# Kernel optimization log

Measured on AMD Instinct MI355X. Metric: run time of the kernel, lower is better.

## Reference

```python
import jax, jax.numpy as jnp
import numpy as np

# Model dims
T0 = 2048      # tokens (batch*seq flattened)
D = 2048       # hidden_size
E = 256        # n_routed_experts
K = 8          # num_experts_per_tok
G = 8          # expert groups
EG = 32        # experts per group
R = 64         # tucker rank
I = 1408       # moe_intermediate_size


def setup_inputs() -> dict:
    key = jax.random.key(0)
    ks = jax.random.split(key, 12)
    f = lambda k, s: jax.random.normal(k, s, dtype=jnp.float32) * 0.02
    return {
        "hidden_states": jax.random.normal(ks[0], (T0, D), dtype=jnp.float32),
        "w_gate": f(ks[1], (D, E)),
        # Tucker factors per group: shared in-factor A, per-expert core C, shared out-factor B
        "A_gate": f(ks[2], (G, D, R)), "C_gate": f(ks[3], (G, EG, R, R)), "B_gate": f(ks[4], (G, R, I)),
        "A_up":   f(ks[5], (G, D, R)), "C_up":   f(ks[6], (G, EG, R, R)), "B_up":   f(ks[7], (G, R, I)),
        "A_down": f(ks[8], (G, I, R)), "C_down": f(ks[9], (G, EG, R, R)), "B_down": f(ks[10], (G, R, D)),
    }


def _tucker(x, A, C, B, inner):
    # x: [T, d_in], A: [d_in, R], C: [EG, R, R] gathered per-token, B: [R, d_out]
    h1 = x @ A                                    # [T, R]
    h2 = jnp.einsum('tr,trs->ts', h1, C[inner])   # per-token expert core
    return h2 @ B                                 # [T, d_out]


def reference(hidden_states, w_gate, A_gate, C_gate, B_gate,
              A_up, C_up, B_up, A_down, C_down, B_down):
    # Router: softmax in fp32, top-k, renormalize
    logits = hidden_states @ w_gate                              # [T0, E]
    probs = jax.nn.softmax(logits.astype(jnp.float32), axis=-1)
    rw, sel = jax.lax.top_k(probs, K)                            # [T0, K]
    rw = (rw / rw.sum(axis=-1, keepdims=True)).astype(hidden_states.dtype)

    idx = sel.reshape(-1)          # [T0*K] expert ids of dispatched rows
    gid = idx // EG                # group id
    inner = idx % EG               # expert within group
    x = jnp.repeat(hidden_states, K, axis=0)   # repeat_interleave dispatch [T0*K, D]

    out = jnp.zeros_like(x)
    for g in range(G):             # static loop over 8 structurally distinct groups
        m = (gid == g)[:, None]
        xg = jnp.where(m, x, 0.0)  # masked dispatch (zeros flow to zero through the MLP)
        go = _tucker(xg, A_gate[g], C_gate[g], B_gate[g], inner)
        uo = _tucker(xg, A_up[g],   C_up[g],   B_up[g],   inner)
        inter = jax.nn.silu(go) * uo
        do = _tucker(inter, A_down[g], C_down[g], B_down[g], inner)
        out = out + jnp.where(m, do, 0.0)

    # weighted combine
    return (out.reshape(T0, K, D) * rw[..., None]).sum(axis=1)
```

## Files before the change

### kernel.cpp

```cpp
#include <hip/hip_runtime.h>
#include <math.h>

constexpr int T0n = 2048;
constexpr int Dn  = 2048;
constexpr int En  = 256;
constexpr int Gn  = 8;
constexpr int EGn = 32;
constexpr int Rn  = 64;
constexpr int In  = 1408;

constexpr int NROWS = T0n * 8;
constexpr int SEGCAP = NROWS;
constexpr int KSPLIT = 4;

typedef __attribute__((ext_vector_type(8))) short s8v;
typedef __attribute__((ext_vector_type(4))) float f4v;
#define MFMA16(a, b, c) __builtin_amdgcn_mfma_f32_16x16x32_bf16(a, b, c, 0, 0, 0)

__device__ __forceinline__ unsigned short f2bf(float x) {
  unsigned int u = __float_as_uint(x);
  unsigned int r = (u + 0x7FFFu + ((u >> 16) & 1u)) >> 16;
  return (unsigned short)r;
}

struct TD { const float* src; unsigned short* dst; int rows, cols, nbx, per_batch, base; };
struct TD6 { TD t[6]; };

__global__ __launch_bounds__(256) void k_tcvt6(TD6 D) {
  __shared__ float tbuf[32][33];
  int id = blockIdx.x;
  int ti = 0;
#pragma unroll
  for (int i = 1; i < 6; ++i) ti = (id >= D.t[i].base) ? i : ti;
  TD d = D.t[ti];
  int local = id - d.base;
  int bz = local / d.per_batch;
  int rem = local - bz * d.per_batch;
  int by = rem / d.nbx;
  int bx = rem - by * d.nbx;

  size_t boff = (size_t)bz * d.rows * d.cols;
  const float* src = d.src + boff;
  unsigned short* dst = d.dst + boff;
  int c0 = bx * 32, r0 = by * 32;
  int tx = threadIdx.x & 31, ty = threadIdx.x >> 5;
  for (int i = ty; i < 32; i += 8)
    tbuf[i][tx] = src[(size_t)(r0 + i) * d.cols + c0 + tx];
  __syncthreads();
  for (int i = ty; i < 32; i += 8)
    dst[(size_t)(c0 + i) * d.rows + r0 + tx] = f2bf(tbuf[tx][i]);
}

__global__ __launch_bounds__(256) void k_router_part(
    const float* __restrict__ A, const float* __restrict__ B,
    double* __restrict__ part, unsigned short* __restrict__ Hb) {
  __shared__ double Asd[32][66];
  __shared__ double Bsd[32][66];
  const int m0 = blockIdx.y * 64, n0 = blockIdx.x * 64;
  const int kbeg = blockIdx.z * (Dn / KSPLIT);
  const int tid = threadIdx.x;
  const int ty = tid >> 4, tx = tid & 15;
  const int lm = tid & 63, lk8 = (tid >> 6) * 8;
  const int br = tid >> 3, bc = (tid & 7) * 8;
  const bool emitH = (blockIdx.x == 0);

  double acc[4][4] = {};

  for (int k0 = kbeg; k0 < kbeg + Dn / KSPLIT; k0 += 32) {
    float4 a0 = *(const float4*)&A[(size_t)(m0 + lm) * Dn + k0 + lk8];
    float4 a1 = *(const float4*)&A[(size_t)(m0 + lm) * Dn + k0 + lk8 + 4];
    Asd[lk8 + 0][lm] = (double)a0.x; Asd[lk8 + 1][lm] = (double)a0.y;
    Asd[lk8 + 2][lm] = (double)a0.z; Asd[lk8 + 3][lm] = (double)a0.w;
    Asd[lk8 + 4][lm] = (double)a1.x; Asd[lk8 + 5][lm] = (double)a1.y;
    Asd[lk8 + 6][lm] = (double)a1.z; Asd[lk8 + 7][lm] = (double)a1.w;
    if (emitH) {
      ushort4 o0, o1;
      o0.x = f2bf(a0.x); o0.y = f2bf(a0.y); o0.z = f2bf(a0.z); o0.w = f2bf(a0.w);
      o1.x = f2bf(a1.x); o1.y = f2bf(a1.y); o1.z = f2bf(a1.z); o1.w = f2bf(a1.w);
      *(ushort4*)&Hb[(size_t)(m0 + lm) * Dn + k0 + lk8] = o0;
      *(ushort4*)&Hb[(size_t)(m0 + lm) * Dn + k0 + lk8 + 4] = o1;
    }
    float4 b0 = *(const float4*)&B[(size_t)(k0 + br) * En + n0 + bc];
    float4 b1 = *(const float4*)&B[(size_t)(k0 + br) * En + n0 + bc + 4];
    Bsd[br][bc + 0] = (double)b0.x; Bsd[br][bc + 1] = (double)b0.y;
    Bsd[br][bc + 2] = (double)b0.z; Bsd[br][bc + 3] = (double)b0.w;
    Bsd[br][bc + 4] = (double)b1.x; Bsd[br][bc + 5] = (double)b1.y;
    Bsd[br][bc + 6] = (double)b1.z; Bsd[br][bc + 7] = (double)b1.w;
    __syncthreads();
#pragma unroll
    for (int kk = 0; kk < 32; ++kk) {
      double a[4], b[4];
#pragma unroll
      for (int i = 0; i < 4; ++i) a[i] = Asd[kk][ty + 16 * i];
#pragma unroll
      for (int j = 0; j < 4; ++j) b[j] = Bsd[kk][tx + 16 * j];
#pragma unroll
      for (int i = 0; i < 4; ++i)
#pragma unroll
        for (int j = 0; j < 4; ++j)
          acc[i][j] += a[i] * b[j];
    }
    __syncthreads();
  }
  double* prow = part + (size_t)blockIdx.z * T0n * En;
#pragma unroll
  for (int i = 0; i < 4; ++i) {
    int row = m0 + ty + 16 * i;
#pragma unroll
    for (int j = 0; j < 4; ++j)
      prow[(size_t)row * En + n0 + tx + 16 * j] = acc[i][j];
  }
}

__global__ __launch_bounds__(256) void k_topk(
    const double* __restrict__ part, int* __restrict__ sel,
    float* __restrict__ rw, int* __restrict__ cnt_e) {
  const int wid = threadIdx.x >> 6, ln = threadIdx.x & 63;
  const int t = blockIdx.x * 4 + wid;

  double v[4];
#pragma unroll
  for (int j = 0; j < 4; ++j) {
    double s = 0.0;
#pragma unroll
    for (int kc = 0; kc < KSPLIT; ++kc)
      s += part[((size_t)kc * T0n + t) * En + ln + 64 * j];
    v[j] = s;
  }

  float topv[8];
  int topi[8];
#pragma unroll
  for (int k = 0; k < 8; ++k) {
    double bv = v[0]; int bi = ln;
#pragma unroll
    for (int j = 1; j < 4; ++j) {
      int cand = ln + 64 * j;
      if (v[j] > bv || (v[j] == bv && cand < bi)) { bv = v[j]; bi = cand; }
    }
#pragma unroll
    for (int off = 32; off > 0; off >>= 1) {
      double ov = __shfl_xor(bv, off);
      int oi = __shfl_xor(bi, off);
      if (ov > bv || (ov == bv && oi < bi)) { bv = ov; bi = oi; }
    }
    topv[k] = (float)bv; topi[k] = bi;
    if ((bi & 63) == ln) v[bi >> 6] = -1e300;
  }

  if (ln < 8) {
    float m = topv[0];
    float ssum = 0.f;
#pragma unroll
    for (int k = 0; k < 8; ++k) ssum += expf(topv[k] - m);
    rw[t * 8 + ln] = expf(topv[ln] - m) / ssum;
    sel[t * 8 + ln] = topi[ln];
    atomicAdd(&cnt_e[topi[ln]], 1);
  }
}

__global__ __launch_bounds__(256) void k_scan(
    const int* __restrict__ cnt_e, int* __restrict__ off_e,
    int* __restrict__ cur_e, int* __restrict__ grp_n) {
  __shared__ int c[256];
  int tid = threadIdx.x;
  c[tid] = cnt_e[tid];
  __syncthreads();
  int g = tid >> 5, ei = tid & 31;
  int run = 0;
  for (int i = 0; i < ei; ++i) run += c[(g << 5) + i];
  off_e[tid] = g * SEGCAP + run;
  cur_e[tid] = g * SEGCAP + run;
  if (ei == 31) grp_n[g] = run + c[tid];
}

__global__ void k_scatter(const int* __restrict__ sel, int* __restrict__ cur_e,
                          int* __restrict__ rseg) {
  int i = blockIdx.x * 256 + threadIdx.x;
  int e = sel[i];
  int pos = atomicAdd(&cur_e[e], 1);
  rseg[pos] = i;
}

__global__ __launch_bounds__(512) void k_h1_mfma(
    const unsigned short* __restrict__ Hb,
    const unsigned short* __restrict__ AgT, const unsigned short* __restrict__ AuT,
    unsigned short* __restrict__ h1gb, unsigned short* __restrict__ h1ub) {
  const int t0 = blockIdx.x * 64;
  const int g = blockIdx.y;
  const unsigned short* Wg = AgT + (size_t)g * Rn * Dn;
  const unsigned short* Wu = AuT + (size_t)g * Rn * Dn;

  __shared__ unsigned short As[64 * 72];
  __shared__ unsigned short Bg_l[64 * 72];
  __shared__ unsigned short Bu_l[64 * 72];
  const int tid = threadIdx.x;
  const int w = tid >> 6, ln = tid & 63;
  const int path = w >> 2, ws = w & 3;
  const int quad = ln >> 4, lane16 = ln & 15;
  const int j = tid >> 3, q = (tid & 7) * 8;

  f4v S[4] = {};

  for (int k0 = 0; k0 < Dn; k0 += 64) {
    *(uint4*)&As[j * 72 + q]   = *(const uint4*)&Hb[(size_t)(t0 + j) * Dn + k0 + q];
    *(uint4*)&Bg_l[j * 72 + q] = *(const uint4*)&Wg[(size_t)j * Dn + k0 + q];
    *(uint4*)&Bu_l[j * 72 + q] = *(const uint4*)&Wu[(size_t)j * Dn + k0 + q];
    __syncthreads();
    const unsigned short* Bl = path ? Bu_l : Bg_l;
#pragma unroll
    for (int kk = 0; kk < 2; ++kk) {
      s8v a = *(const s8v*)&As[(ws * 16 + lane16) * 72 + kk * 32 + quad * 8];
#pragma unroll
      for (int nt = 0; nt < 4; ++nt) {
        s8v b = *(const s8v*)&Bl[(nt * 16 + lane16) * 72 + kk * 32 + quad * 8];
        S[nt] = MFMA16(a, b, S[nt]);
      }
    }
    __syncthreads();
  }
  unsigned short* out = path ? h1ub : h1gb;
#pragma unroll
  for (int nt = 0; nt < 4; ++nt)
#pragma unroll
    for (int r = 0; r < 4; ++r) {
      int row = t0 + ws * 16 + quad * 4 + r;
      int col = g * 64 + nt * 16 + lane16;
      out[(size_t)row * (Gn * Rn) + col] = f2bf(S[nt][r]);
    }
}

__global__ __launch_bounds__(512) void k_core_gu(
    const unsigned short* __restrict__ h1gb, const unsigned short* __restrict__ h1ub,
    const float* __restrict__ Cgate, const float* __restrict__ Cup,
    const int* __restrict__ rseg, const int* __restrict__ off_e,
    const int* __restrict__ cnt_e,
    unsigned short* __restrict__ h2gb, unsigned short* __restrict__ h2ub) {
  const int e = blockIdx.x;
  const int ne = cnt_e[e];
  if (ne == 0) return;
  const int g = e >> 5;
  const int base = off_e[e];
  __shared__ unsigned short Cg_l[64 * 72];
  __shared__ unsigned short Cu_l[64 * 72];
  __shared__ unsigned short Ags[64 * 72];
  __shared__ unsigned short Aus[64 * 72];
  __shared__ int rids[64];
  const int tid = threadIdx.x;
  const int w = tid >> 6, ln = tid & 63;
  const int path = w >> 2, ws = w & 3;
  const int quad = ln >> 4, lane16 = ln & 15;
  const int j = tid >> 3, q = (tid & 7) * 8;
  {
    const float* cg = Cgate + (size_t)e * (Rn * Rn);
    const float* cu = Cup   + (size_t)e * (Rn * Rn);
    float4 g0 = *(const float4*)&cg[j * 64 + q];
    float4 g1 = *(const float4*)&cg[j * 64 + q + 4];
    float4 u0 = *(const float4*)&cu[j * 64 + q];
    float4 u1 = *(const float4*)&cu[j * 64 + q + 4];
    Cg_l[(q + 0) * 72 + j] = f2bf(g0.x); Cg_l[(q + 1) * 72 + j] = f2bf(g0.y);
    Cg_l[(q + 2) * 72 + j] = f2bf(g0.z); Cg_l[(q + 3) * 72 + j] = f2bf(g0.w);
    Cg_l[(q + 4) * 72 + j] = f2bf(g1.x); Cg_l[(q + 5) * 72 + j] = f2bf(g1.y);
    Cg_l[(q + 6) * 72 + j] = f2bf(g1.z); Cg_l[(q + 7) * 72 + j] = f2bf(g1.w);
    Cu_l[(q + 0) * 72 + j] = f2bf(u0.x); Cu_l[(q + 1) * 72 + j] = f2bf(u0.y);
    Cu_l[(q + 2) * 72 + j] = f2bf(u0.z); Cu_l[(q + 3) * 72 + j] = f2bf(u0.w);
    Cu_l[(q + 4) * 72 + j] = f2bf(u1.x); Cu_l[(q + 5) * 72 + j] = f2bf(u1.y);
    Cu_l[(q + 6) * 72 + j] = f2bf(u1.z); Cu_l[(q + 7) * 72 + j] = f2bf(u1.w);
  }
  const int ntile = (ne + 63) >> 6;
  for (int it = 0; it < ntile; ++it) {
    int mi = it * 64 + j;
    int rid = (mi < ne) ? rseg[base + mi] : -1;
    if ((tid & 7) == 0) rids[j] = rid;
    uint4 zg = {0, 0, 0, 0}, zu = {0, 0, 0, 0};
    if (rid >= 0) {
      zg = *(const uint4*)&h1gb[(size_t)(rid >> 3) * (Gn * Rn) + g * 64 + q];
      zu = *(const uint4*)&h1ub[(size_t)(rid >> 3) * (Gn * Rn) + g * 64 + q];
    }
    *(uint4*)&Ags[j * 72 + q] = zg;
    *(uint4*)&Aus[j * 72 + q] = zu;
    __syncthreads();
    const unsigned short* Al = path ? Aus : Ags;
    const unsigned short* Cl = path ? Cu_l : Cg_l;
    f4v S[4] = {};
#pragma unroll
    for (int kk = 0; kk < 2; ++kk) {
      s8v a = *(const s8v*)&Al[(ws * 16 + lane16) * 72 + kk * 32 + quad * 8];
#pragma unroll
      for (int nt = 0; nt < 4; ++nt) {
        s8v b = *(const s8v*)&Cl[(nt * 16 + lane16) * 72 + kk * 32 + quad * 8];
        S[nt] = MFMA16(a, b, S[nt]);
      }
    }
    unsigned short* out = path ? h2ub : h2gb;
#pragma unroll
    for (int nt = 0; nt < 4; ++nt)
#pragma unroll
      for (int r = 0; r < 4; ++r) {
        int rid2 = rids[ws * 16 + quad * 4 + r];
        if (rid2 >= 0)
          out[(size_t)rid2 * 64 + nt * 16 + lane16] = f2bf(S[nt][r]);
      }
    __syncthreads();
  }
}

__global__ __launch_bounds__(256) void k_expand_mfma(
    const unsigned short* __restrict__ h2gb, const unsigned short* __restrict__ h2ub,
    const unsigned short* __restrict__ BgT, const unsigned short* __restrict__ BuT,
    const unsigned short* __restrict__ AdT,
    const int* __restrict__ rseg, const int* __restrict__ grp_n,
    float* __restrict__ h1d) {
  const int g = blockIdx.z;
  const int ng = grp_n[g];
  const int m0 = blockIdx.y * 128;
  if (m0 >= ng) return;
  const int c_beg = blockIdx.x * 6;
  const int c_end = min(22, c_beg + 6);

  __shared__ unsigned short Hg_l[128 * 72];
  __shared__ unsigned short Hu_l[128 * 72];
  __shared__ unsigned short Bg_l[64 * 72];
  __shared__ unsigned short Bu_l[64 * 72];
  __shared__ unsigned short Ad_l[64 * 72];
  __shared__ int rids[128];

  const int tid = threadIdx.x;
  const int w = tid >> 6, ln = tid & 63;
  const int quad = ln >> 4, lane16 = ln & 15;

  if (tid < 128) rids[tid] = (m0 + tid < ng) ? rseg[g * SEGCAP + m0 + tid] : -1;
  __syncthreads();
#pragma unroll
  for (int i = 0; i < 4; ++i) {
    int c = tid + i * 256;
    int row = c >> 3, cc = (c & 7) * 8;
    int rid = rids[row];
    uint4 zg = {0, 0, 0, 0}, zu = {0, 0, 0, 0};
    if (rid >= 0) {
      zg = *(const uint4*)&h2gb[(size_t)rid * 64 + cc];
      zu = *(const uint4*)&h2ub[(size_t)rid * 64 + cc];
    }
    *(uint4*)&Hg_l[row * 72 + cc] = zg;
    *(uint4*)&Hu_l[row * 72 + cc] = zu;
  }

  const unsigned short* Bg_base = BgT + (size_t)g * In * Rn;
  const unsigned short* Bu_base = BuT + (size_t)g * In * Rn;
  const unsigned short* Ad_base = AdT + (size_t)g * Rn * In;

  f4v P[2][4] = {};

  for (int c = c_beg; c < c_end; ++c) {
    const int i0 = c * 64;
#pragma unroll
    for (int i = 0; i < 2; ++i) {
      int cq = tid + i * 256;
      int row = cq >> 3, co = (cq & 7) * 8;
      *(uint4*)&Bg_l[row * 72 + co] = *(const uint4*)&Bg_base[(size_t)(i0 + row) * Rn + co];
      *(uint4*)&Bu_l[row * 72 + co] = *(const uint4*)&Bu_base[(size_t)(i0 + row) * Rn + co];
      *(uint4*)&Ad_l[row * 72 + co] = *(const uint4*)&Ad_base[(size_t)row * In + i0 + co];
    }
    __syncthreads();

    f4v Sg[2][4] = {}, Su[2][4] = {};
#pragma unroll
    for (int kk = 0; kk < 2; ++kk) {
      s8v ag[2], au[2], bg[4], bu[4];
#pragma unroll
      for (int mt = 0; mt < 2; ++mt) {
        ag[mt] = *(const s8v*)&Hg_l[(w * 32 + mt * 16 + lane16) * 72 + kk * 32 + quad * 8];
        au[mt] = *(const s8v*)&Hu_l[(w * 32 + mt * 16 + lane16) * 72 + kk * 32 + quad * 8];
      }
#pragma unroll
      for (int nt = 0; nt < 4; ++nt) {
        bg[nt] = *(const s8v*)&Bg_l[(nt * 16 + lane16) * 72 + kk * 32 + quad * 8];
        bu[nt] = *(const s8v*)&Bu_l[(nt * 16 + lane16) * 72 + kk * 32 + quad * 8];
      }
#pragma unroll
      for (int mt = 0; mt < 2; ++mt)
#pragma unroll
        for (int nt = 0; nt < 4; ++nt) {
          Sg[mt][nt] = MFMA16(ag[mt], bg[nt], Sg[mt][nt]);
          Su[mt][nt] = MFMA16(au[mt], bu[nt], Su[mt][nt]);
        }
    }
    __syncthreads();
    {
      unsigned short* ibuf = (w < 2) ? Bg_l : Bu_l;
#pragma unroll
      for (int mt = 0; mt < 2; ++mt)
#pragma unroll
        for (int nt = 0; nt < 4; ++nt)
#pragma unroll
          for (int r = 0; r < 4; ++r) {
            float sg = Sg[mt][nt][r];
            float v = sg / (1.f + __expf(-sg)) * Su[mt][nt][r];
            int row = (w * 32 + mt * 16 + quad * 4 + r) & 63;
            ibuf[row * 72 + nt * 16 + lane16] = f2bf(v);
          }
    }
    __syncthreads();
#pragma unroll
    for (int kk = 0; kk < 2; ++kk) {
      s8v ai[2], bd[4];
#pragma unroll
      for (int mt = 0; mt < 2; ++mt) {
        const unsigned short* src = (w < 2) ? Bg_l : Bu_l;
        int arow = (w * 32 + mt * 16 + lane16) & 63;
        ai[mt] = *(const s8v*)&src[arow * 72 + kk * 32 + quad * 8];
      }
#pragma unroll
      for (int nt = 0; nt < 4; ++nt)
        bd[nt] = *(const s8v*)&Ad_l[(nt * 16 + lane16) * 72 + kk * 32 + quad * 8];
#pragma unroll
      for (int mt = 0; mt < 2; ++mt)
#pragma unroll
        for (int nt = 0; nt < 4; ++nt)
          P[mt][nt] = MFMA16(ai[mt], bd[nt], P[mt][nt]);
    }
    __syncthreads();
  }

#pragma unroll
  for (int mt = 0; mt < 2; ++mt)
#pragma unroll
    for (int nt = 0; nt < 4; ++nt)
#pragma unroll
      for (int r = 0; r < 4; ++r) {
        int lrow = w * 32 + mt * 16 + quad * 4 + r;
        int rid = rids[lrow];
        if (rid >= 0)
          atomicAdd(&h1d[(size_t)rid * 64 + nt * 16 + lane16], P[mt][nt][r]);
      }
}

__global__ __launch_bounds__(512) void k_core_down(
    const float* __restrict__ h1d, const float* __restrict__ Cdown,
    const float* __restrict__ rw,
    const int* __restrict__ rseg, const int* __restrict__ off_e,
    const int* __restrict__ cnt_e,
    float* __restrict__ y) {
  const int e = blockIdx.x;
  const int ne = cnt_e[e];
  if (ne == 0) return;
  const int g = e >> 5;
  const int base = off_e[e];
  __shared__ unsigned short Bd_l[64 * 72];
  __shared__ unsigned short Ad_l[128 * 72];
  __shared__ int rids[128];
  const int tid = threadIdx.x;
  const int w = tid >> 6, ln = tid & 63;
  const int quad = ln >> 4, lane16 = ln & 15;
  {
    int j = tid >> 3, q = (tid & 7) * 8;
    const float* cd = Cdown + (size_t)e * (Rn * Rn);
    float4 d0 = *(const float4*)&cd[j * 64 + q];
    float4 d1 = *(const float4*)&cd[j * 64 + q + 4];
    Bd_l[(q + 0) * 72 + j] = f2bf(d0.x); Bd_l[(q + 1) * 72 + j] = f2bf(d0.y);
    Bd_l[(q + 2) * 72 + j] = f2bf(d0.z); Bd_l[(q + 3) * 72 + j] = f2bf(d0.w);
    Bd_l[(q + 4) * 72 + j] = f2bf(d1.x); Bd_l[(q + 5) * 72 + j] = f2bf(d1.y);
    Bd_l[(q + 6) * 72 + j] = f2bf(d1.z); Bd_l[(q + 7) * 72 + j] = f2bf(d1.w);
  }
  const int gj = tid >> 2, gq = (tid & 3) * 16;
  const int ntile = (ne + 127) >> 7;
  for (int it = 0; it < ntile; ++it) {
    int mi = it * 128 + gj;
    int rid = (mi < ne) ? rseg[base + mi] : -1;
    if ((tid & 3) == 0) rids[gj] = rid;
#pragma unroll
    for (int i = 0; i < 4; ++i) {
      int kb = gq + i * 4;
      float4 vd = {0.f, 0.f, 0.f, 0.f};
      if (rid >= 0) vd = *(const float4*)&h1d[(size_t)rid * 64 + kb];
      ushort4 od;
      od.x = f2bf(vd.x); od.y = f2bf(vd.y); od.z = f2bf(vd.z); od.w = f2bf(vd.w);
      *(ushort4*)&Ad_l[gj * 72 + kb] = od;
    }
    __syncthreads();
    f4v Sd[4] = {};
#pragma unroll
    for (int kk = 0; kk < 2; ++kk) {
      s8v ad = *(const s8v*)&Ad_l[(w * 16 + lane16) * 72 + kk * 32 + quad * 8];
#pragma unroll
      for (int nt = 0; nt < 4; ++nt) {
        s8v bd = *(const s8v*)&Bd_l[(nt * 16 + lane16) * 72 + kk * 32 + quad * 8];
        Sd[nt] = MFMA16(ad, bd, Sd[nt]);
      }
    }
#pragma unroll
    for (int nt = 0; nt < 4; ++nt)
#pragma unroll
      for (int r = 0; r < 4; ++r) {
        int rid2 = rids[w * 16 + quad * 4 + r];
        if (rid2 >= 0) {
          float wgt = rw[rid2];
          atomicAdd(&y[(size_t)(rid2 >> 3) * (Gn * Rn) + g * 64 + nt * 16 + lane16],
                    wgt * Sd[nt][r]);
        }
      }
    __syncthreads();
  }
}

__global__ __launch_bounds__(256) void k_combine(
    const float* __restrict__ y, const unsigned short* __restrict__ BdT,
    float* __restrict__ outp) {
  const int t0 = blockIdx.y * 128, n0 = blockIdx.x * 128;
  __shared__ unsigned short As[128 * 72];
  __shared__ unsigned short Bs[128 * 72];
  const int tid = threadIdx.x;
  const int w = tid >> 6, ln = tid & 63;
  const int quad = ln >> 4, lane16 = ln & 15;
  const int mbase = (w >> 1) * 64, nbase = (w & 1) * 64;

  f4v acc[4][4] = {};

  for (int k0 = 0; k0 < Gn * Rn; k0 += 64) {
#pragma unroll
    for (int i = 0; i < 8; ++i) {
      int c = tid + i * 256;
      int row = c >> 4, cc = (c & 15) * 4;
      float4 v = *(const float4*)&y[(size_t)(t0 + row) * (Gn * Rn) + k0 + cc];
      ushort4 o;
      o.x = f2bf(v.x); o.y = f2bf(v.y); o.z = f2bf(v.z); o.w = f2bf(v.w);
      *(ushort4*)&As[row * 72 + cc] = o;
    }
#pragma unroll
    for (int i = 0; i < 4; ++i) {
      int c = tid + i * 256;
      int row = c >> 3, cc = (c & 7) * 8;
      *(uint4*)&Bs[row * 72 + cc] = *(const uint4*)&BdT[(size_t)(n0 + row) * (Gn * Rn) + k0 + cc];
    }
    __syncthreads();
#pragma unroll
    for (int kk = 0; kk < 2; ++kk) {
      s8v a[4], b[4];
#pragma unroll
      for (int mt = 0; mt < 4; ++mt)
        a[mt] = *(const s8v*)&As[(mbase + mt * 16 + lane16) * 72 + kk * 32 + quad * 8];
#pragma unroll
      for (int nt = 0; nt < 4; ++nt)
        b[nt] = *(const s8v*)&Bs[(nbase + nt * 16 + lane16) * 72 + kk * 32 + quad * 8];
#pragma unroll
      for (int mt = 0; mt < 4; ++mt)
#pragma unroll
        for (int nt = 0; nt < 4; ++nt)
          acc[mt][nt] = MFMA16(a[mt], b[nt], acc[mt][nt]);
    }
    __syncthreads();
  }
#pragma unroll
  for (int mt = 0; mt < 4; ++mt)
#pragma unroll
    for (int nt = 0; nt < 4; ++nt)
#pragma unroll
      for (int r = 0; r < 4; ++r)
        outp[(size_t)(t0 + mbase + mt * 16 + quad * 4 + r) * Dn +
             n0 + nbase + nt * 16 + lane16] = acc[mt][nt][r];
}

extern "C" void kernel_launch(void* const* d_in, const int* in_sizes, int n_in,
                              void* d_out, int out_size, void* d_ws, size_t ws_size,
                              hipStream_t stream) {
  const float* hidden = (const float*)d_in[0];
  const float* w_gate = (const float*)d_in[1];
  const float* A_gate = (const float*)d_in[2];
  const float* C_gate = (const float*)d_in[3];
  const float* B_gate = (const float*)d_in[4];
  const float* A_up   = (const float*)d_in[5];
  const float* C_up   = (const float*)d_in[6];
  const float* B_up   = (const float*)d_in[7];
  const float* A_down = (const float*)d_in[8];
  const float* C_down = (const float*)d_in[9];
  const float* B_down = (const float*)d_in[10];
  float* out = (float*)d_out;

  char* base = (char*)d_ws;
  double* part = (double*)d_ws;
  size_t o = 0;
  unsigned short* h2gb = (unsigned short*)(base + o); o += (size_t)NROWS * Rn * 2;
  unsigned short* h2ub = (unsigned short*)(base + o); o += (size_t)NROWS * Rn * 2;
  unsigned short* h1gb = (unsigned short*)(base + o); o += (size_t)T0n * Gn * Rn * 2;
  unsigned short* h1ub = (unsigned short*)(base + o); o += (size_t)T0n * Gn * Rn * 2;
  float* h1d = (float*)(base + o); o += (size_t)NROWS * Rn * 4;
  float* y   = (float*)(base + o); o += (size_t)T0n * Gn * Rn * 4;
  unsigned short* Hb  = (unsigned short*)(base + o); o += (size_t)T0n * Dn * 2;
  unsigned short* AgT = (unsigned short*)(base + o); o += (size_t)Gn * Rn * Dn * 2;
  unsigned short* AuT = (unsigned short*)(base + o); o += (size_t)Gn * Rn * Dn * 2;
  unsigned short* BgT = (unsigned short*)(base + o); o += (size_t)Gn * In * Rn * 2;
  unsigned short* BuT = (unsigned short*)(base + o); o += (size_t)Gn * In * Rn * 2;
  unsigned short* AdT = (unsigned short*)(base + o); o += (size_t)Gn * Rn * In * 2;
  unsigned short* BdT = (unsigned short*)(base + o); o += (size_t)Dn * Gn * Rn * 2;
  float* rwp = (float*)(base + o); o += (size_t)NROWS * 4;
  int* sel   = (int*)(base + o); o += (size_t)NROWS * 4;
  int* rseg  = (int*)(base + o); o += (size_t)Gn * SEGCAP * 4;
  int* cnt_e = (int*)(base + o); o += En * 4;
  int* off_e = (int*)(base + o); o += En * 4;
  int* cur_e = (int*)(base + o); o += En * 4;
  int* grp_n = (int*)(base + o); o += Gn * 4;

  hipMemsetAsync(cnt_e, 0, En * sizeof(int), stream);

  k_router_part<<<dim3(En / 64, T0n / 64, KSPLIT), 256, 0, stream>>>(
      hidden, w_gate, part, Hb);
  k_topk<<<T0n / 4, 256, 0, stream>>>(part, sel, rwp, cnt_e);
  k_scan<<<1, 256, 0, stream>>>(cnt_e, off_e, cur_e, grp_n);
  k_scatter<<<NROWS / 256, 256, 0, stream>>>(sel, cur_e, rseg);

  hipMemsetAsync(h1d, 0, (size_t)(NROWS * Rn + T0n * Gn * Rn) * sizeof(float), stream);

  {
    TD6 D;
    D.t[0] = {A_gate, AgT, Dn, Rn, Rn / 32, (Rn / 32) * (Dn / 32), 0};
    D.t[1] = {A_up,   AuT, Dn, Rn, Rn / 32, (Rn / 32) * (Dn / 32), 1024};
    D.t[2] = {B_gate, BgT, Rn, In, In / 32, (In / 32) * (Rn / 32), 2048};
    D.t[3] = {B_up,   BuT, Rn, In, In / 32, (In / 32) * (Rn / 32), 2752};
    D.t[4] = {A_down, AdT, In, Rn, Rn / 32, (Rn / 32) * (In / 32), 3456};
    D.t[5] = {B_down, BdT, Gn * Rn, Dn, Dn / 32, (Dn / 32) * (Gn * Rn / 32), 4160};
    k_tcvt6<<<5184, 256, 0, stream>>>(D);
  }

  k_h1_mfma<<<dim3(T0n / 64, Gn), 512, 0, stream>>>(Hb, AgT, AuT, h1gb, h1ub);
  k_core_gu<<<En, 512, 0, stream>>>(h1gb, h1ub, C_gate, C_up,
                                    rseg, off_e, cnt_e, h2gb, h2ub);
  k_expand_mfma<<<dim3(4, NROWS / 128, Gn), 256, 0, stream>>>(
      h2gb, h2ub, BgT, BuT, AdT, rseg, grp_n, h1d);
  k_core_down<<<En, 512, 0, stream>>>(h1d, C_down, rwp,
                                      rseg, off_e, cnt_e, y);
  k_combine<<<dim3(Dn / 128, T0n / 128), 256, 0, stream>>>(y, BdT, out);
}
```

Baseline: 354.3 us.

## Use float LDS tiles in router GEMM, double K-split, drop expand split-K atomics

The router GEMM now stages fp32 tiles in LDS, reads them as float4 and converts to double in registers. Each thread owns a contiguous 4x4 output block, stored as double2, and KSPLIT doubles to 8 for more parallelism. The expand kernel no longer splits the intermediate dimension across four blocks, so it writes h1d directly instead of using atomicAdd, and the h1d memset goes away. The workspace is rearranged so the larger partial buffer overlaps earlier regions. The cost is fewer, longer expand blocks and twice the partial-sum traffic in topk.

```diff
diff --git a/kernel.cpp b/kernel.cpp
--- a/kernel.cpp
+++ b/kernel.cpp
@@ -11,7 +11,7 @@
 
 constexpr int NROWS = T0n * 8;
 constexpr int SEGCAP = NROWS;
-constexpr int KSPLIT = 4;
+constexpr int KSPLIT = 8;
 
 typedef __attribute__((ext_vector_type(8))) short s8v;
 typedef __attribute__((ext_vector_type(4))) float f4v;
@@ -54,10 +54,11 @@
 __global__ __launch_bounds__(256) void k_router_part(
     const float* __restrict__ A, const float* __restrict__ B,
     double* __restrict__ part, unsigned short* __restrict__ Hb) {
-  __shared__ double Asd[32][66];
-  __shared__ double Bsd[32][66];
+  __shared__ float As[32][68];
+  __shared__ float Bs[32][68];
   const int m0 = blockIdx.y * 64, n0 = blockIdx.x * 64;
-  const int kbeg = blockIdx.z * (Dn / KSPLIT);
+  const int kc = blockIdx.z;
+  const int kbeg = kc * (Dn / KSPLIT);
   const int tid = threadIdx.x;
   const int ty = tid >> 4, tx = tid & 15;
   const int lm = tid & 63, lk8 = (tid >> 6) * 8;
@@ -69,10 +70,10 @@
   for (int k0 = kbeg; k0 < kbeg + Dn / KSPLIT; k0 += 32) {
     float4 a0 = *(const float4*)&A[(size_t)(m0 + lm) * Dn + k0 + lk8];
     float4 a1 = *(const float4*)&A[(size_t)(m0 + lm) * Dn + k0 + lk8 + 4];
-    Asd[lk8 + 0][lm] = (double)a0.x; Asd[lk8 + 1][lm] = (double)a0.y;
-    Asd[lk8 + 2][lm] = (double)a0.z; Asd[lk8 + 3][lm] = (double)a0.w;
-    Asd[lk8 + 4][lm] = (double)a1.x; Asd[lk8 + 5][lm] = (double)a1.y;
-    Asd[lk8 + 6][lm] = (double)a1.z; Asd[lk8 + 7][lm] = (double)a1.w;
+    As[lk8 + 0][lm] = a0.x; As[lk8 + 1][lm] = a0.y;
+    As[lk8 + 2][lm] = a0.z; As[lk8 + 3][lm] = a0.w;
+    As[lk8 + 4][lm] = a1.x; As[lk8 + 5][lm] = a1.y;
+    As[lk8 + 6][lm] = a1.z; As[lk8 + 7][lm] = a1.w;
     if (emitH) {
       ushort4 o0, o1;
       o0.x = f2bf(a0.x); o0.y = f2bf(a0.y); o0.z = f2bf(a0.z); o0.w = f2bf(a0.w);
@@ -80,20 +81,15 @@
       *(ushort4*)&Hb[(size_t)(m0 + lm) * Dn + k0 + lk8] = o0;
       *(ushort4*)&Hb[(size_t)(m0 + lm) * Dn + k0 + lk8 + 4] = o1;
     }
-    float4 b0 = *(const float4*)&B[(size_t)(k0 + br) * En + n0 + bc];
-    float4 b1 = *(const float4*)&B[(size_t)(k0 + br) * En + n0 + bc + 4];
-    Bsd[br][bc + 0] = (double)b0.x; Bsd[br][bc + 1] = (double)b0.y;
-    Bsd[br][bc + 2] = (double)b0.z; Bsd[br][bc + 3] = (double)b0.w;
-    Bsd[br][bc + 4] = (double)b1.x; Bsd[br][bc + 5] = (double)b1.y;
-    Bsd[br][bc + 6] = (double)b1.z; Bsd[br][bc + 7] = (double)b1.w;
+    *(float4*)&Bs[br][bc]     = *(const float4*)&B[(size_t)(k0 + br) * En + n0 + bc];
+    *(float4*)&Bs[br][bc + 4] = *(const float4*)&B[(size_t)(k0 + br) * En + n0 + bc + 4];
     __syncthreads();
 #pragma unroll
     for (int kk = 0; kk < 32; ++kk) {
-      double a[4], b[4];
-#pragma unroll
-      for (int i = 0; i < 4; ++i) a[i] = Asd[kk][ty + 16 * i];
-#pragma unroll
-      for (int j = 0; j < 4; ++j) b[j] = Bsd[kk][tx + 16 * j];
+      float4 af = *(const float4*)&As[kk][ty * 4];
+      float4 bf = *(const float4*)&Bs[kk][tx * 4];
+      double a[4] = {(double)af.x, (double)af.y, (double)af.z, (double)af.w};
+      double b[4] = {(double)bf.x, (double)bf.y, (double)bf.z, (double)bf.w};
 #pragma unroll
       for (int i = 0; i < 4; ++i)
 #pragma unroll
@@ -102,13 +98,17 @@
     }
     __syncthreads();
   }
-  double* prow = part + (size_t)blockIdx.z * T0n * En;
+  double* prow = part + (size_t)kc * T0n * En;
 #pragma unroll
   for (int i = 0; i < 4; ++i) {
-    int row = m0 + ty + 16 * i;
-#pragma unroll
-    for (int j = 0; j < 4; ++j)
-      prow[(size_t)row * En + n0 + tx + 16 * j] = acc[i][j];
+    int row = m0 + ty * 4 + i;
+#pragma unroll
+    for (int j2 = 0; j2 < 2; ++j2) {
+      double2 dv;
+      dv.x = acc[i][j2 * 2 + 0];
+      dv.y = acc[i][j2 * 2 + 1];
+      *(double2*)&prow[(size_t)row * En + n0 + tx * 4 + j2 * 2] = dv;
+    }
   }
 }
 
@@ -311,12 +311,10 @@
     const unsigned short* __restrict__ AdT,
     const int* __restrict__ rseg, const int* __restrict__ grp_n,
     float* __restrict__ h1d) {
-  const int g = blockIdx.z;
+  const int g = blockIdx.y;
   const int ng = grp_n[g];
-  const int m0 = blockIdx.y * 128;
+  const int m0 = blockIdx.x * 128;
   if (m0 >= ng) return;
-  const int c_beg = blockIdx.x * 6;
-  const int c_end = min(22, c_beg + 6);
 
   __shared__ unsigned short Hg_l[128 * 72];
   __shared__ unsigned short Hu_l[128 * 72];
@@ -351,7 +349,7 @@
 
   f4v P[2][4] = {};
 
-  for (int c = c_beg; c < c_end; ++c) {
+  for (int c = 0; c < 22; ++c) {
     const int i0 = c * 64;
 #pragma unroll
     for (int i = 0; i < 2; ++i) {
@@ -431,7 +429,7 @@
         int lrow = w * 32 + mt * 16 + quad * 4 + r;
         int rid = rids[lrow];
         if (rid >= 0)
-          atomicAdd(&h1d[(size_t)rid * 64 + nt * 16 + lane16], P[mt][nt][r]);
+          h1d[(size_t)rid * 64 + nt * 16 + lane16] = P[mt][nt][r];
       }
 }
 
@@ -585,16 +583,17 @@
   unsigned short* h1ub = (unsigned short*)(base + o); o += (size_t)T0n * Gn * Rn * 2;
   float* h1d = (float*)(base + o); o += (size_t)NROWS * Rn * 4;
   float* y   = (float*)(base + o); o += (size_t)T0n * Gn * Rn * 4;
-  unsigned short* Hb  = (unsigned short*)(base + o); o += (size_t)T0n * Dn * 2;
   unsigned short* AgT = (unsigned short*)(base + o); o += (size_t)Gn * Rn * Dn * 2;
   unsigned short* AuT = (unsigned short*)(base + o); o += (size_t)Gn * Rn * Dn * 2;
   unsigned short* BgT = (unsigned short*)(base + o); o += (size_t)Gn * In * Rn * 2;
   unsigned short* BuT = (unsigned short*)(base + o); o += (size_t)Gn * In * Rn * 2;
   unsigned short* AdT = (unsigned short*)(base + o); o += (size_t)Gn * Rn * In * 2;
   unsigned short* BdT = (unsigned short*)(base + o); o += (size_t)Dn * Gn * Rn * 2;
+  int* rseg  = (int*)(base + o); o += (size_t)Gn * SEGCAP * 4;
+  o = (size_t)KSPLIT * T0n * En * 8;
+  unsigned short* Hb  = (unsigned short*)(base + o); o += (size_t)T0n * Dn * 2;
   float* rwp = (float*)(base + o); o += (size_t)NROWS * 4;
   int* sel   = (int*)(base + o); o += (size_t)NROWS * 4;
-  int* rseg  = (int*)(base + o); o += (size_t)Gn * SEGCAP * 4;
   int* cnt_e = (int*)(base + o); o += En * 4;
   int* off_e = (int*)(base + o); o += En * 4;
   int* cur_e = (int*)(base + o); o += En * 4;
@@ -608,7 +607,7 @@
   k_scan<<<1, 256, 0, stream>>>(cnt_e, off_e, cur_e, grp_n);
   k_scatter<<<NROWS / 256, 256, 0, stream>>>(sel, cur_e, rseg);
 
-  hipMemsetAsync(h1d, 0, (size_t)(NROWS * Rn + T0n * Gn * Rn) * sizeof(float), stream);
+  hipMemsetAsync(y, 0, (size_t)T0n * Gn * Rn * sizeof(float), stream);
 
   {
     TD6 D;
@@ -624,7 +623,7 @@
   k_h1_mfma<<<dim3(T0n / 64, Gn), 512, 0, stream>>>(Hb, AgT, AuT, h1gb, h1ub);
   k_core_gu<<<En, 512, 0, stream>>>(h1gb, h1ub, C_gate, C_up,
                                     rseg, off_e, cnt_e, h2gb, h2ub);
-  k_expand_mfma<<<dim3(4, NROWS / 128, Gn), 256, 0, stream>>>(
+  k_expand_mfma<<<dim3(NROWS / 128, Gn), 256, 0, stream>>>(
       h2gb, h2ub, BgT, BuT, AdT, rseg, grp_n, h1d);
   k_core_down<<<En, 512, 0, stream>>>(h1d, C_down, rwp,
                                       rseg, off_e, cnt_e, y);
```

New measurement: 375.5 us. 1.06x slower.
